# Optimization experiments

Measured on AMD Instinct MI355X. Metric: run time of the kernel, lower is better.

The kernel has to match this reference:

```python
import jax, jax.numpy as jnp
import numpy as np

B, N, D = 4, 1024, 1024
H, DH = 16, 64
N_LAYERS = 3  # len(mlp_dims) - 1 with implicit_mlp_hiddens=(64, 64)
EPS = 1.1920929e-07  # torch.nn.RMSNorm default eps = finfo(float32).eps


def _rope_tables(n, dtype):
    # lucidrains RotaryEmbedding: theta=10000, interleaved freq repeat
    inv_freq = 1.0 / (10000.0 ** (np.arange(0, DH, 2, dtype=np.float64) / DH))
    t = np.arange(n, dtype=np.float64)[:, None] * inv_freq[None, :]  # [n, DH/2]
    t = np.repeat(t, 2, axis=-1)  # [n, DH], freqs interleaved (f0,f0,f1,f1,...)
    return jnp.asarray(np.cos(t), dtype), jnp.asarray(np.sin(t), dtype)


def _rope_rotate(x, cos, sin):
    # x: [b,h,n,d]; rotate_half on interleaved pairs: (x1,x2) -> (-x2,x1)
    xp = x.reshape(*x.shape[:-1], DH // 2, 2)
    xr = jnp.stack((-xp[..., 1], xp[..., 0]), axis=-1).reshape(x.shape)
    return x * cos + xr * sin


def _attend(q, k, v):
    # rotate_queries_with_cached_keys with no cache: same positions for q and k
    n = q.shape[-2]
    cos, sin = _rope_tables(n, q.dtype)
    q = _rope_rotate(q, cos, sin)
    k = _rope_rotate(k, cos, sin)
    scale = DH ** -0.5
    scores = jnp.einsum('bhqd,bhkd->bhqk', q, k) * scale
    causal = jnp.tril(jnp.ones((n, n), dtype=bool))
    scores = jnp.where(causal, scores, -jnp.inf)
    attn = jax.nn.softmax(scores, axis=-1)
    return jnp.einsum('bhqk,bhkd->bhqd', attn, v)


def _split_heads(x):
    b, n, _ = x.shape
    return x.reshape(b, n, H, DH).transpose(0, 2, 1, 3)  # b h n d


def setup_inputs() -> dict:
    key = jax.random.key(0)
    ks = jax.random.split(key, 6)
    s = 0.02
    return {
        'tokens': jax.random.normal(ks[0], (B, N, D), jnp.float32),
        'gamma': jnp.ones((D,), jnp.float32),                                  # RMSNorm weight
        'Wq': jax.random.normal(ks[1], (D, H * DH), jnp.float32) * s,           # to_queries
        'Wk': jax.random.normal(ks[2], (N_LAYERS, D, H * DH), jnp.float32) * s, # stacked key projections
        'Wv': jax.random.normal(ks[3], (N_LAYERS, D, H * DH), jnp.float32) * s, # stacked value projections
        'Wo': jax.random.normal(ks[4], (H * DH, D), jnp.float32) * s,           # to_out
    }


def reference(tokens, gamma, Wq, Wk, Wv, Wo):
    b, n, d = tokens.shape
    # RMSNorm (prenorm)
    x = tokens * jax.lax.rsqrt(jnp.mean(tokens * tokens, axis=-1, keepdims=True) + EPS) * gamma
    out = _split_heads(x @ Wq)  # queries, [b h n d]
    for i in range(N_LAYERS):
        k = _split_heads(x @ Wk[i])
        v = _split_heads(x @ Wv[i])
        out = _attend(out, k, v)
        if i < N_LAYERS - 1:
            out = jax.nn.silu(out)  # implicit MLP activation between attention stages
    out = out.transpose(0, 2, 1, 3).reshape(b, n, H * DH)  # merge heads
    return out @ Wo
```

## Files before the change

### kernel.cpp

```cpp
#include <hip/hip_runtime.h>


typedef unsigned short u16;
typedef short s16x8 __attribute__((ext_vector_type(8)));
typedef u16 u16x4 __attribute__((ext_vector_type(4)));
typedef float f32x4 __attribute__((ext_vector_type(4)));

typedef __attribute__((address_space(1))) const unsigned int as1c_uint;
typedef __attribute__((address_space(3))) unsigned int as3_uint;

__device__ __forceinline__ float b2f(u16 h) {
  union { unsigned int u; float f; } v; v.u = ((unsigned int)h) << 16; return v.f;
}
__device__ __forceinline__ u16 f2b(float f) {
  union { float f; unsigned int u; } v; v.f = f;
  return (u16)((v.u + 0x7FFFu + ((v.u >> 16) & 1u)) >> 16);
}
__device__ __forceinline__ void gload16(const u16* g, const u16* lds) {
  __builtin_amdgcn_global_load_lds((as1c_uint*)(size_t)g,
                                   (as3_uint*)(unsigned int)(size_t)lds, 16, 0, 0);
}

__global__ __launch_bounds__(256)
void rmsnorm_kernel(const float* __restrict__ T, const float* __restrict__ gamma,
                    u16* __restrict__ X) {
  const int row = blockIdx.x, tid = threadIdx.x;
  const float4 v = ((const float4*)(T + (size_t)row * 1024))[tid];
  float ss = v.x * v.x + v.y * v.y + v.z * v.z + v.w * v.w;
#pragma unroll
  for (int msk = 1; msk <= 32; msk <<= 1) ss += __shfl_xor(ss, msk, 64);
  __shared__ float red[4];
  if ((tid & 63) == 0) red[tid >> 6] = ss;
  __syncthreads();
  const float tot = red[0] + red[1] + red[2] + red[3];
  const float r = rsqrtf(tot * (1.0f / 1024.0f) + 1.1920929e-07f);
  const float4 gm = ((const float4*)gamma)[tid];
  u16x4 o;
  o[0] = f2b(v.x * r * gm.x); o[1] = f2b(v.y * r * gm.y);
  o[2] = f2b(v.z * r * gm.z); o[3] = f2b(v.w * r * gm.w);
  *(u16x4*)(X + (size_t)row * 1024 + tid * 4) = o;
}

__global__ __launch_bounds__(256)
void rope_kernel(float* __restrict__ ct, float* __restrict__ st) {
  const int idx = blockIdx.x * 256 + threadIdx.x;
  const int n = idx >> 5, j = idx & 31;
  const double freq = pow(10000.0, -(double)j / 32.0);
  const double a = (double)n * freq;
  ct[idx] = (float)cos(a);
  st[idx] = (float)sin(a);
}

__global__ __launch_bounds__(256)
void ropek_kernel(u16* __restrict__ K, const float* __restrict__ ct,
                  const float* __restrict__ st) {
  u16* row = K + (size_t)blockIdx.y * 4194304 + (size_t)blockIdx.x * 1024;
  const int n = blockIdx.x & 1023;
  const int t = threadIdx.x;
  const int j = ((t * 4) & 63) >> 1;
  const float2 c2 = *(const float2*)(ct + n * 32 + j);
  const float2 s2 = *(const float2*)(st + n * 32 + j);
  u16x4 v = *(u16x4*)(row + t * 4);
  const float x0 = b2f(v[0]), x1 = b2f(v[1]);
  const float y0 = b2f(v[2]), y1 = b2f(v[3]);
  u16x4 o;
  o[0] = f2b(x0 * c2.x - x1 * s2.x);
  o[1] = f2b(x1 * c2.x + x0 * s2.x);
  o[2] = f2b(y0 * c2.y - y1 * s2.y);
  o[3] = f2b(y1 * c2.y + y0 * s2.y);
  *(u16x4*)(row + t * 4) = o;
}

__global__ __launch_bounds__(256)
void transw_kernel(const float* __restrict__ Wq, const float* __restrict__ Wk,
                   const float* __restrict__ Wv, const float* __restrict__ Wo,
                   u16* __restrict__ wt) {
  __shared__ float tile[32][33];
  const int z = blockIdx.z;
  const float* src = (z == 0) ? Wq
                   : (z <= 3) ? (Wk + (size_t)(z - 1) * 1048576)
                   : (z <= 6) ? (Wv + (size_t)(z - 4) * 1048576)
                              : Wo;
  u16* dst = wt + (size_t)z * 1048576;
  const int tx = threadIdx.x & 31, ty = threadIdx.x >> 5;
  const int bx = blockIdx.x * 32, by = blockIdx.y * 32;
#pragma unroll
  for (int i = 0; i < 4; ++i)
    tile[ty + i * 8][tx] = src[(size_t)(by + ty + i * 8) * 1024 + bx + tx];
  __syncthreads();
#pragma unroll
  for (int i = 0; i < 4; ++i)
    dst[(size_t)(bx + ty + i * 8) * 1024 + by + tx] = f2b(tile[tx][ty + i * 8]);
}

template <int KIND>
__global__ __launch_bounds__(256)
void gemm_kernel(const u16* __restrict__ A, const u16* __restrict__ Bt,
                 void* __restrict__ Cout) {
  const int z = blockIdx.z;
  const int tid = threadIdx.x;
  const int w = tid >> 6, l = tid & 63;
  const int g = l >> 4, ll = l & 15;
  const int wr = w >> 1, wc = w & 1;
  const int m0 = blockIdx.y * 128, n0 = blockIdx.x * 128;

  const u16* Ab;
  const u16* Bb;
  if (KIND == 0) {
    Ab = A + (size_t)m0 * 1024;
    Bb = Bt + (size_t)z * 1048576 + (size_t)n0 * 1024;
  } else {
    Ab = A + (size_t)m0 * 1024 + z * 512;
    Bb = Bt + (size_t)n0 * 1024 + z * 512;
  }

  __shared__ u16 SH[4][4096];

  const f32x4 zero = {0.f, 0.f, 0.f, 0.f};
  f32x4 acc[4][4];
#pragma unroll
  for (int i = 0; i < 4; ++i)
#pragma unroll
    for (int j = 0; j < 4; ++j) acc[i][j] = zero;

  const int sr = l >> 2;
  const int sc = (l & 3) * 8;

  auto stage = [&](int buf, int t) {
    const int k0 = t * 32;
#pragma unroll
    for (int j = 0; j < 2; ++j) {
      const int seg = j * 4 + w;
      const int r = seg * 16 + sr;
      gload16(Ab + (size_t)r * 1024 + k0 + sc, &SH[buf][seg * 512]);
      gload16(Bb + (size_t)r * 1024 + k0 + sc, &SH[2 + buf][seg * 512]);
    }
  };

  const int NT = (KIND == 1) ? 16 : 32;
  stage(0, 0);
  __syncthreads();
  int buf = 0;
  for (int t = 0; t < NT; ++t) {
    if (t < NT - 1) stage(buf ^ 1, t + 1);
    s16x8 af[4], bfr[4];
#pragma unroll
    for (int mf = 0; mf < 4; ++mf)
      af[mf] = *(const s16x8*)&SH[buf][(wr * 64 + mf * 16 + ll) * 32 + g * 8];
#pragma unroll
    for (int nf = 0; nf < 4; ++nf)
      bfr[nf] = *(const s16x8*)&SH[2 + buf][(wc * 64 + nf * 16 + ll) * 32 + g * 8];
#pragma unroll
    for (int mf = 0; mf < 4; ++mf)
#pragma unroll
      for (int nf = 0; nf < 4; ++nf)
        acc[mf][nf] = __builtin_amdgcn_mfma_f32_16x16x32_bf16(af[mf], bfr[nf],
                                                              acc[mf][nf], 0, 0, 0);
    __syncthreads();
    buf ^= 1;
  }

  if (KIND == 0) {
    u16* C = (u16*)Cout + (size_t)z * 4194304;
    if (z < 4) {
      u16* T = &SH[0][0];
#pragma unroll
      for (int mf = 0; mf < 4; ++mf)
#pragma unroll
        for (int nf = 0; nf < 4; ++nf) {
          const int c = wc * 64 + nf * 16 + ll;
#pragma unroll
          for (int rg = 0; rg < 4; ++rg) {
            const int r = wr * 64 + mf * 16 + g * 4 + rg;
            T[r * 128 + (c ^ ((r & 7) << 4))] = f2b(acc[mf][nf][rg]);
          }
        }
      __syncthreads();
#pragma unroll
      for (int i = 0; i < 8; ++i) {
        const int R = (tid >> 4) + i * 16;
        const int c0 = (tid & 15) * 8;
        const s16x8 v = *(const s16x8*)&T[R * 128 + (c0 ^ ((R & 7) << 4))];
        *(s16x8*)&C[(size_t)(m0 + R) * 1024 + n0 + c0] = v;
      }
    } else {
#pragma unroll
      for (int mf = 0; mf < 4; ++mf)
#pragma unroll
        for (int nf = 0; nf < 4; ++nf) {
          const int col = n0 + wc * 64 + nf * 16 + ll;
          const int hh = col >> 6, d = col & 63;
          const int mb = m0 + wr * 64 + mf * 16 + g * 4;
          const int bb = mb >> 10, n = mb & 1023;
          u16x4 pk;
#pragma unroll
          for (int rg = 0; rg < 4; ++rg) pk[rg] = f2b(acc[mf][nf][rg]);
          *(u16x4*)&C[((size_t)((bb * 16 + hh) * 64 + d)) * 1024 + n] = pk;
        }
    }
  } else {
    float* C = (float*)Cout + (size_t)z * 4194304;
#pragma unroll
    for (int mf = 0; mf < 4; ++mf)
#pragma unroll
      for (int nf = 0; nf < 4; ++nf) {
        const int col = n0 + wc * 64 + nf * 16 + ll;
#pragma unroll
        for (int rg = 0; rg < 4; ++rg) {
          const int m = m0 + wr * 64 + mf * 16 + g * 4 + rg;
          C[(size_t)m * 1024 + col] = acc[mf][nf][rg];
        }
      }
  }
}

__global__ __launch_bounds__(256)
void reduce_kernel(const float* __restrict__ P, float* __restrict__ out) {
  const int i = (blockIdx.x * 256 + threadIdx.x) * 4;
  const float4 a = *(const float4*)(P + i);
  const float4 b = *(const float4*)(P + 4194304 + i);
  float4 o;
  o.x = a.x + b.x; o.y = a.y + b.y; o.z = a.z + b.z; o.w = a.w + b.w;
  *(float4*)(out + i) = o;
}

template <int SILU>
__global__ __launch_bounds__(256)
void attn_kernel(const u16* __restrict__ Q, const u16* __restrict__ K,
                 const u16* __restrict__ Vt, u16* __restrict__ O,
                 const float* __restrict__ ct, const float* __restrict__ st) {
  const int lin = blockIdx.x + (blockIdx.y << 3);
  const int role = (lin & 7) * 64 + (lin >> 3);
  const int p = role & 7, bh = role >> 3;
  const int q_lo = p, q_hi = 15 - p;
  const int b = bh >> 4, h = bh & 15;
  const int tid = threadIdx.x, w = tid >> 6, l = tid & 63;
  const int g = l >> 4, ll = l & 15;

  const u16* Qb = Q + (size_t)(b * 1024) * 1024 + h * 64;
  const u16* Kb = K + (size_t)(b * 1024) * 1024 + h * 64;
  const u16* Vb = Vt + (size_t)((b * 16 + h) * 64) * 1024;
  u16* Ob = O + (size_t)(b * 1024) * 1024 + h * 64;

  __shared__ u16 Ksh[2][64 * 72];
  __shared__ u16 Psh[4][16 * 72];

  s16x8 qfL[2], qfH[2];
  auto loadQ = [&](int qt, s16x8* qf) {
    const int qrow = qt * 64 + w * 16 + ll;
#pragma unroll
    for (int kc = 0; kc < 2; ++kc) {
      const int d0 = kc * 32 + g * 8;
      const int j0 = d0 >> 1;
      const float4 c4 = *(const float4*)(ct + qrow * 32 + j0);
      const float4 s4v = *(const float4*)(st + qrow * 32 + j0);
      const s16x8 qin = *(const s16x8*)(Qb + (size_t)qrow * 1024 + d0);
      s16x8 qo;
#pragma unroll
      for (int pp = 0; pp < 4; ++pp) {
        const float c = ((const float*)&c4)[pp], s = ((const float*)&s4v)[pp];
        const float x0 = b2f((u16)qin[2 * pp]), x1 = b2f((u16)qin[2 * pp + 1]);
        qo[2 * pp]     = (short)f2b((x0 * c - x1 * s) * 0.125f);
        qo[2 * pp + 1] = (short)f2b((x1 * c + x0 * s) * 0.125f);
      }
      qf[kc] = qo;
    }
  };
  loadQ(q_lo, qfL);
  loadQ(q_hi, qfH);

  float mL[4], lsL[4], mH[4], lsH[4];
  f32x4 oL[4], oH[4];
  const f32x4 zero = {0.f, 0.f, 0.f, 0.f};
#pragma unroll
  for (int rg = 0; rg < 4; ++rg) {
    mL[rg] = -3.0e38f; lsL[rg] = 0.f; mH[rg] = -3.0e38f; lsH[rg] = 0.f;
  }
#pragma unroll
  for (int df = 0; df < 4; ++df) { oL[df] = zero; oH[df] = zero; }

  const int srow = tid >> 2;
  const int sc0 = (tid & 3) * 16;

  s16x8 kr0, kr1;
  auto kload = [&](int t) {
    const u16* kp = Kb + (size_t)(t * 64 + srow) * 1024 + sc0;
    kr0 = *(const s16x8*)kp;
    kr1 = *(const s16x8*)(kp + 8);
  };
  auto kstore = [&](int bf) {
    *(s16x8*)&Ksh[bf][srow * 72 + sc0] = kr0;
    *(s16x8*)&Ksh[bf][srow * 72 + sc0 + 8] = kr1;
  };

  kload(0);
  kstore(0);
  __syncthreads();
  int buf = 0;

  for (int t = 0; t <= q_hi; ++t) {
    const bool pre = (t < q_hi);
    if (pre) kload(t + 1);

    s16x8 vb[2][4];
#pragma unroll
    for (int kc = 0; kc < 2; ++kc)
#pragma unroll
      for (int df = 0; df < 4; ++df)
        vb[kc][df] = *(const s16x8*)(Vb + (size_t)(df * 16 + ll) * 1024 +
                                     t * 64 + kc * 32 + g * 8);

    auto process = [&](const s16x8* qf, float* mm, float* ls, f32x4* o,
                       bool diag) {
      f32x4 s4[4];
      __builtin_amdgcn_s_setprio(1);
#pragma unroll
      for (int nf = 0; nf < 4; ++nf) {
        const s16x8 kb0 = *(const s16x8*)&Ksh[buf][(nf * 16 + ll) * 72 + g * 8];
        const s16x8 kb1 = *(const s16x8*)&Ksh[buf][(nf * 16 + ll) * 72 + 32 + g * 8];
        f32x4 sv = zero;
        sv = __builtin_amdgcn_mfma_f32_16x16x32_bf16(qf[0], kb0, sv, 0, 0, 0);
        sv = __builtin_amdgcn_mfma_f32_16x16x32_bf16(qf[1], kb1, sv, 0, 0, 0);
        s4[nf] = sv;
      }
      __builtin_amdgcn_s_setprio(0);

      if (diag) {
#pragma unroll
        for (int nf = 0; nf < 4; ++nf)
#pragma unroll
          for (int rg = 0; rg < 4; ++rg)
            if (nf * 16 + ll > w * 16 + g * 4 + rg) s4[nf][rg] = -3.0e38f;
      }

#pragma unroll
      for (int rg = 0; rg < 4; ++rg) {
        float rmax = fmaxf(fmaxf(s4[0][rg], s4[1][rg]),
                           fmaxf(s4[2][rg], s4[3][rg]));
        rmax = fmaxf(rmax, __shfl_xor(rmax, 1, 64));
        rmax = fmaxf(rmax, __shfl_xor(rmax, 2, 64));
        rmax = fmaxf(rmax, __shfl_xor(rmax, 4, 64));
        rmax = fmaxf(rmax, __shfl_xor(rmax, 8, 64));
        const float mn = fmaxf(mm[rg], rmax);
        const float scl = __expf(mm[rg] - mn);
        mm[rg] = mn;
        float ps = 0.f;
#pragma unroll
        for (int nf = 0; nf < 4; ++nf) {
          const float pv = __expf(s4[nf][rg] - mn);
          s4[nf][rg] = pv;
          ps += pv;
        }
        ls[rg] = ls[rg] * scl + ps;
#pragma unroll
        for (int df = 0; df < 4; ++df) o[df][rg] *= scl;
      }

#pragma unroll
      for (int nf = 0; nf < 4; ++nf)
#pragma unroll
        for (int rg = 0; rg < 4; ++rg)
          Psh[w][(g * 4 + rg) * 72 + nf * 16 + ll] = f2b(s4[nf][rg]);

      __builtin_amdgcn_s_setprio(1);
#pragma unroll
      for (int kc = 0; kc < 2; ++kc) {
        const s16x8 pa = *(const s16x8*)&Psh[w][ll * 72 + kc * 32 + g * 8];
#pragma unroll
        for (int df = 0; df < 4; ++df)
          o[df] = __builtin_amdgcn_mfma_f32_16x16x32_bf16(pa, vb[kc][df],
                                                          o[df], 0, 0, 0);
      }
      __builtin_amdgcn_s_setprio(0);
    };

    process(qfH, mH, lsH, oH, t == q_hi);
    if (t <= q_lo) process(qfL, mL, lsL, oL, t == q_lo);

    if (pre) kstore(buf ^ 1);
    __syncthreads();
    buf ^= 1;
  }

  auto finish = [&](float* ls, f32x4* o, int qt) {
#pragma unroll
    for (int rg = 0; rg < 4; ++rg) {
      float v = ls[rg];
      v += __shfl_xor(v, 1, 64);
      v += __shfl_xor(v, 2, 64);
      v += __shfl_xor(v, 4, 64);
      v += __shfl_xor(v, 8, 64);
      ls[rg] = 1.f / v;
    }
#pragma unroll
    for (int df = 0; df < 4; ++df)
#pragma unroll
      for (int rg = 0; rg < 4; ++rg) {
        float val = o[df][rg] * ls[rg];
        if (SILU) val = val / (1.f + __expf(-val));
        Ob[(size_t)(qt * 64 + w * 16 + g * 4 + rg) * 1024 + df * 16 + ll] =
            f2b(val);
      }
  };
  finish(lsH, oH, q_hi);
  finish(lsL, oL, q_lo);
}

extern "C" void kernel_launch(void* const* d_in, const int* in_sizes, int n_in,
                              void* d_out, int out_size, void* d_ws, size_t ws_size,
                              hipStream_t stream) {
  (void)in_sizes; (void)n_in; (void)out_size; (void)ws_size;
  const float* tokens = (const float*)d_in[0];
  const float* gamma  = (const float*)d_in[1];
  const float* Wq     = (const float*)d_in[2];
  const float* Wk     = (const float*)d_in[3];
  const float* Wv     = (const float*)d_in[4];
  const float* Wo     = (const float*)d_in[5];
  float* out = (float*)d_out;

  u16* x    = (u16*)d_ws;
  u16* wt   = x + (size_t)4096 * 1024;
  u16* qkv  = wt + (size_t)8 * 1048576;
  u16* outA = qkv + (size_t)7 * 4194304;
  u16* outB = outA + 4194304;
  float* ct = (float*)(outB + 4194304);
  float* st = ct + 32768;
  float* Pp = (float*)(qkv + 1 * 4194304);

  rmsnorm_kernel<<<4096, 256, 0, stream>>>(tokens, gamma, x);
  rope_kernel<<<128, 256, 0, stream>>>(ct, st);
  transw_kernel<<<dim3(32, 32, 8), 256, 0, stream>>>(Wq, Wk, Wv, Wo, wt);
  gemm_kernel<0><<<dim3(8, 32, 7), 256, 0, stream>>>(x, wt, qkv);

  const size_t M4 = 4194304;
  ropek_kernel<<<dim3(4096, 3), 256, 0, stream>>>(qkv + M4, ct, st);

  attn_kernel<1><<<dim3(8, 64), 256, 0, stream>>>(qkv, qkv + 1 * M4, qkv + 4 * M4,
                                                  outA, ct, st);
  attn_kernel<1><<<dim3(8, 64), 256, 0, stream>>>(outA, qkv + 2 * M4, qkv + 5 * M4,
                                                  outB, ct, st);
  attn_kernel<0><<<dim3(8, 64), 256, 0, stream>>>(outB, qkv + 3 * M4, qkv + 6 * M4,
                                                  outA, ct, st);

  gemm_kernel<1><<<dim3(8, 32, 2), 256, 0, stream>>>(outA, wt + (size_t)7 * 1048576,
                                                     (void*)Pp);
  reduce_kernel<<<4096, 256, 0, stream>>>(Pp, out);
}
```

Measured before the change: 262.7 us.

## Deepen GEMM LDS pipeline to four stages with XOR swizzle and setprio

Replaces the double-buffered K-loop in the projection GEMM with a four-slot ring, issuing global-to-LDS loads three tiles ahead and gating each step on explicit vmcnt waits plus a single barrier. It also XOR-swizzles the 16-byte column chunks in LDS to reduce bank conflicts on fragment reads, and raises wave priority around the MFMA block. The goal is to hide global load latency and cut LDS conflicts, at the cost of doubling shared memory per block (64 KB), which may lower occupancy.

```diff
diff --git a/kernel.cpp b/kernel.cpp
--- a/kernel.cpp
+++ b/kernel.cpp
@@ -114,7 +114,7 @@
     Bb = Bt + (size_t)n0 * 1024 + z * 512;
   }
 
-  __shared__ u16 SH[4][4096];
+  __shared__ u16 SH[4][8192];
 
   const f32x4 zero = {0.f, 0.f, 0.f, 0.f};
   f32x4 acc[4][4];
@@ -123,42 +123,58 @@
 #pragma unroll
     for (int j = 0; j < 4; ++j) acc[i][j] = zero;
 
-  const int sr = l >> 2;
-  const int sc = (l & 3) * 8;
-
-  auto stage = [&](int buf, int t) {
-    const int k0 = t * 32;
-#pragma unroll
-    for (int j = 0; j < 2; ++j) {
-      const int seg = j * 4 + w;
-      const int r = seg * 16 + sr;
-      gload16(Ab + (size_t)r * 1024 + k0 + sc, &SH[buf][seg * 512]);
-      gload16(Bb + (size_t)r * 1024 + k0 + sc, &SH[2 + buf][seg * 512]);
+  auto stage = [&](int t2) {
+    const int slot = t2 & 3;
+    const int k0 = t2 * 32;
+#pragma unroll
+    for (int c = 0; c < 2; ++c) {
+      const int chunk = c * 4 + w;
+      const int row = chunk * 16 + (l >> 2);
+      const int sl = l & 3;
+      const int kk = k0 + ((sl ^ ((row >> 1) & 3)) << 3);
+      gload16(Ab + (size_t)row * 1024 + kk, &SH[slot][chunk * 512]);
+      gload16(Bb + (size_t)row * 1024 + kk, &SH[slot][4096 + chunk * 512]);
     }
   };
 
   const int NT = (KIND == 1) ? 16 : 32;
-  stage(0, 0);
-  __syncthreads();
-  int buf = 0;
+  stage(0); stage(1); stage(2);
+
+#pragma unroll
   for (int t = 0; t < NT; ++t) {
-    if (t < NT - 1) stage(buf ^ 1, t + 1);
+    const int beyond = (NT - 1) - t;
+    if (beyond >= 2)      asm volatile("s_waitcnt vmcnt(8)" ::: "memory");
+    else if (beyond == 1) asm volatile("s_waitcnt vmcnt(4)" ::: "memory");
+    else                  asm volatile("s_waitcnt vmcnt(0)" ::: "memory");
+    __builtin_amdgcn_s_barrier();
+
+    const int slot = t & 3;
+    const u16* As = &SH[slot][0];
+    const u16* Bs = &SH[slot][4096];
     s16x8 af[4], bfr[4];
 #pragma unroll
-    for (int mf = 0; mf < 4; ++mf)
-      af[mf] = *(const s16x8*)&SH[buf][(wr * 64 + mf * 16 + ll) * 32 + g * 8];
-#pragma unroll
-    for (int nf = 0; nf < 4; ++nf)
-      bfr[nf] = *(const s16x8*)&SH[2 + buf][(wc * 64 + nf * 16 + ll) * 32 + g * 8];
+    for (int mf = 0; mf < 4; ++mf) {
+      const int row = wr * 64 + mf * 16 + ll;
+      af[mf] = *(const s16x8*)&As[row * 32 + ((g ^ ((row >> 1) & 3)) << 3)];
+    }
+#pragma unroll
+    for (int nf = 0; nf < 4; ++nf) {
+      const int row = wc * 64 + nf * 16 + ll;
+      bfr[nf] = *(const s16x8*)&Bs[row * 32 + ((g ^ ((row >> 1) & 3)) << 3)];
+    }
+
+    if (t + 3 < NT) stage(t + 3);
+
+    __builtin_amdgcn_s_setprio(1);
 #pragma unroll
     for (int mf = 0; mf < 4; ++mf)
 #pragma unroll
       for (int nf = 0; nf < 4; ++nf)
         acc[mf][nf] = __builtin_amdgcn_mfma_f32_16x16x32_bf16(af[mf], bfr[nf],
                                                               acc[mf][nf], 0, 0, 0);
-    __syncthreads();
-    buf ^= 1;
+    __builtin_amdgcn_s_setprio(0);
   }
+  __syncthreads();
 
   if (KIND == 0) {
     u16* C = (u16*)Cout + (size_t)z * 4194304;
```

Result: faster. 254.0 us (-3.3%).
